# Performance work log

Hardware: AMD Instinct MI355X
Metric: run time of the kernel (lower is better)

Reference implementation:

```python
import jax, jax.numpy as jnp
import numpy as np

MIN_DISTANCE = 1.0  # default forward arg of the torch module


def setup_inputs() -> dict:
    key = jax.random.key(0)
    k1, k2 = jax.random.split(key)
    B, N = 4, 4096
    coords = jax.random.normal(k1, (B, N, 3), dtype=jnp.float32) * 5.0
    steric_radii = jax.random.uniform(k2, (B, N), dtype=jnp.float32)
    return {"coords": coords, "steric_radii": steric_radii}


def reference(coords, steric_radii):
    # coords: [B,N,3], steric_radii: [B,N]
    diff = coords[:, :, None, :] - coords[:, None, :, :]          # [B,N,N,3]
    d2 = jnp.sum(diff * diff, axis=-1)                             # [B,N,N]
    # safe sqrt: exact 0 on the diagonal (matches torch.cdist), no NaN grads
    pairwise = jnp.where(d2 > 0, jnp.sqrt(jnp.where(d2 > 0, d2, 1.0)), 0.0)
    sr = steric_radii[:, :, None] + steric_radii[:, None, :]       # [B,N,N]
    target = jnp.maximum(MIN_DISTANCE, sr)
    penalty = jax.nn.relu(target - pairwise)[..., None]            # [B,N,N,1]
    direction = jnp.clip(diff, -1.0, 1.0)                          # [B,N,N,3]
    adjustment = jnp.mean(penalty * direction, axis=2)             # [B,N,3]
    return coords + 0.1 * adjustment
```

## Files before the change

kernel.cpp:

```cpp
#include <hip/hip_runtime.h>

#define BB 4
#define NN 4096
#define TPB 1024
#define IBL 32
#define STREAMS 64
#define JPS (NN / STREAMS)
#define GRP 4

#if __has_builtin(__builtin_amdgcn_sqrtf)
  #define FAST_SQRT __builtin_amdgcn_sqrtf
#else
  #define FAST_SQRT sqrtf
#endif

__device__ __forceinline__ float clip1(float x) {
    return fminf(fmaxf(x, -1.0f), 1.0f);
}

__global__ __launch_bounds__(TPB, 8) void ncp_one(
    const float* __restrict__ coords,
    const float* __restrict__ radii,
    float* __restrict__ out)
{
    __shared__ __align__(16) char smem[81920];
    float4* pts = (float4*)smem;
    float*  rad = (float*)(smem + 65536);
    float*  red = (float*)smem;

    const int b = blockIdx.z;
    const int ibase = blockIdx.x * IBL;

    for (int p = threadIdx.x; p < NN; p += TPB) {
        const int g = b * NN + p;
        const float x = coords[3 * g + 0];
        const float y = coords[3 * g + 1];
        const float z = coords[3 * g + 2];
        pts[p] = make_float4(x, y, z, fmaf(z, z, fmaf(y, y, x * x)));
        rad[p] = radii[g];
    }
    __syncthreads();

    const int l = threadIdx.x & 63;
    const int li = l & 15;
    const int q  = l >> 4;
    const int w  = threadIdx.x >> 6;
    const int stream = w * 4 + q;
    const int jbase = stream * JPS;

    const float4 me0 = pts[ibase + li];
    const float4 me1 = pts[ibase + 16 + li];
    const float ri0 = rad[ibase + li];
    const float ri1 = rad[ibase + 16 + li];
    const float m2x0 = -2.0f * me0.x, m2y0 = -2.0f * me0.y, m2z0 = -2.0f * me0.z;
    const float m2x1 = -2.0f * me1.x, m2y1 = -2.0f * me1.y, m2z1 = -2.0f * me1.z;
    const float n20 = me0.w, n21 = me1.w;
    const float thr0 = (1.0f + ri0) * (1.0f + ri0) - n20;
    const float thr1 = (1.0f + ri1) * (1.0f + ri1) - n21;

    float ax0 = 0.0f, ay0 = 0.0f, az0 = 0.0f;
    float ax1 = 0.0f, ay1 = 0.0f, az1 = 0.0f;

    for (int k0 = 0; k0 < JPS; k0 += GRP) {
        float4 c[GRP];
        #pragma unroll
        for (int g = 0; g < GRP; ++g)
            c[g] = pts[jbase + k0 + g];
        #pragma unroll
        for (int g = 0; g < GRP; ++g) {
            const float sd0 = fmaf(m2z0, c[g].z,
                              fmaf(m2y0, c[g].y, fmaf(m2x0, c[g].x, c[g].w)));
            const float sd1 = fmaf(m2z1, c[g].z,
                              fmaf(m2y1, c[g].y, fmaf(m2x1, c[g].x, c[g].w)));
            if (__any(sd0 < thr0)) {
                const float rj   = rad[jbase + k0 + g];
                const float dist = FAST_SQRT(fmaxf(sd0 + n20, 0.0f));
                const float tgt  = fmaxf(1.0f, ri0 + rj);
                const float p    = fmaxf(tgt - dist, 0.0f);
                const float dx   = me0.x - c[g].x;
                const float dy   = me0.y - c[g].y;
                const float dz   = me0.z - c[g].z;
                ax0 = fmaf(p, clip1(dx), ax0);
                ay0 = fmaf(p, clip1(dy), ay0);
                az0 = fmaf(p, clip1(dz), az0);
            }
            if (__any(sd1 < thr1)) {
                const float rj   = rad[jbase + k0 + g];
                const float dist = FAST_SQRT(fmaxf(sd1 + n21, 0.0f));
                const float tgt  = fmaxf(1.0f, ri1 + rj);
                const float p    = fmaxf(tgt - dist, 0.0f);
                const float dx   = me1.x - c[g].x;
                const float dy   = me1.y - c[g].y;
                const float dz   = me1.z - c[g].z;
                ax1 = fmaf(p, clip1(dx), ax1);
                ay1 = fmaf(p, clip1(dy), ay1);
                az1 = fmaf(p, clip1(dz), az1);
            }
        }
    }

    __syncthreads();
    {
        const int r0 = (stream * IBL + li) * 3;
        const int r1 = (stream * IBL + 16 + li) * 3;
        red[r0 + 0] = ax0; red[r0 + 1] = ay0; red[r0 + 2] = az0;
        red[r1 + 0] = ax1; red[r1 + 1] = ay1; red[r1 + 2] = az1;
    }
    __syncthreads();

    if (threadIdx.x < IBL * 3) {
        float acc = 0.0f;
        #pragma unroll
        for (int s = 0; s < STREAMS; ++s)
            acc += red[s * (IBL * 3) + threadIdx.x];
        const int o = (b * NN + ibase) * 3 + threadIdx.x;
        out[o] = fmaf(0.1f / (float)NN, acc, coords[o]);
    }
}

extern "C" void kernel_launch(void* const* d_in, const int* in_sizes, int n_in,
                              void* d_out, int out_size, void* d_ws, size_t ws_size,
                              hipStream_t stream) {
    const float* coords = (const float*)d_in[0];
    const float* radii  = (const float*)d_in[1];
    float* out = (float*)d_out;
    (void)d_ws; (void)ws_size;

    ncp_one<<<dim3(NN / IBL, 1, BB), TPB, 0, stream>>>(coords, radii, out);
}
```

Before: 69.66 us.

## Register-block four i-points per thread with strided j-streams across 128 streams

Each thread now holds four i-points (8 lanes × 4) instead of two, and the j range is split into 128 interleaved streams with stride-128 access rather than contiguous chunks. Every j-point load from shared memory is reused across more i-points, and the 8 lanes of a group read the same address so the value is broadcast. The reduction buffer uses a padded stride of 100 to reduce LDS bank conflicts, and the direction vector is rebuilt from the -2x coefficients so the raw i coordinates need not stay in registers. The costs are more registers per thread, more partial sums to reduce, and coarser wave-wide __any branches, since each now covers 8 i-points × 8 streams.

```diff
diff --git a/kernel.cpp b/kernel.cpp
--- a/kernel.cpp
+++ b/kernel.cpp
@@ -4,9 +4,11 @@
 #define NN 4096
 #define TPB 1024
 #define IBL 32
-#define STREAMS 64
-#define JPS (NN / STREAMS)
-#define GRP 4
+#define IPT 4
+#define STREAMS 128
+#define JPT (NN / STREAMS)
+#define GRP 2
+#define RSTRIDE 100
 
 #if __has_builtin(__builtin_amdgcn_sqrtf)
   #define FAST_SQRT __builtin_amdgcn_sqrtf
@@ -41,80 +43,76 @@
     }
     __syncthreads();
 
-    const int l = threadIdx.x & 63;
-    const int li = l & 15;
-    const int q  = l >> 4;
+    const int l  = threadIdx.x & 63;
+    const int li = l & 7;
+    const int o  = l >> 3;
     const int w  = threadIdx.x >> 6;
-    const int stream = w * 4 + q;
-    const int jbase = stream * JPS;
+    const int s  = w * 8 + o;
 
-    const float4 me0 = pts[ibase + li];
-    const float4 me1 = pts[ibase + 16 + li];
-    const float ri0 = rad[ibase + li];
-    const float ri1 = rad[ibase + 16 + li];
-    const float m2x0 = -2.0f * me0.x, m2y0 = -2.0f * me0.y, m2z0 = -2.0f * me0.z;
-    const float m2x1 = -2.0f * me1.x, m2y1 = -2.0f * me1.y, m2z1 = -2.0f * me1.z;
-    const float n20 = me0.w, n21 = me1.w;
-    const float thr0 = (1.0f + ri0) * (1.0f + ri0) - n20;
-    const float thr1 = (1.0f + ri1) * (1.0f + ri1) - n21;
+    float m2x[IPT], m2y[IPT], m2z[IPT], thr[IPT], ri[IPT];
+    float ax[IPT], ay[IPT], az[IPT];
+    #pragma unroll
+    for (int t = 0; t < IPT; ++t) {
+        const float4 me = pts[ibase + li + 8 * t];
+        const float  r  = rad[ibase + li + 8 * t];
+        m2x[t] = -2.0f * me.x;
+        m2y[t] = -2.0f * me.y;
+        m2z[t] = -2.0f * me.z;
+        ri[t]  = r;
+        thr[t] = (1.0f + r) * (1.0f + r) - me.w;
+        ax[t] = 0.0f; ay[t] = 0.0f; az[t] = 0.0f;
+    }
 
-    float ax0 = 0.0f, ay0 = 0.0f, az0 = 0.0f;
-    float ax1 = 0.0f, ay1 = 0.0f, az1 = 0.0f;
+    const float4* __restrict__ pj = pts + s;
+    const float*  __restrict__ rj = rad + s;
 
-    for (int k0 = 0; k0 < JPS; k0 += GRP) {
+    for (int k0 = 0; k0 < JPT; k0 += GRP) {
         float4 c[GRP];
         #pragma unroll
         for (int g = 0; g < GRP; ++g)
-            c[g] = pts[jbase + k0 + g];
+            c[g] = pj[(k0 + g) * STREAMS];
         #pragma unroll
         for (int g = 0; g < GRP; ++g) {
-            const float sd0 = fmaf(m2z0, c[g].z,
-                              fmaf(m2y0, c[g].y, fmaf(m2x0, c[g].x, c[g].w)));
-            const float sd1 = fmaf(m2z1, c[g].z,
-                              fmaf(m2y1, c[g].y, fmaf(m2x1, c[g].x, c[g].w)));
-            if (__any(sd0 < thr0)) {
-                const float rj   = rad[jbase + k0 + g];
-                const float dist = FAST_SQRT(fmaxf(sd0 + n20, 0.0f));
-                const float tgt  = fmaxf(1.0f, ri0 + rj);
-                const float p    = fmaxf(tgt - dist, 0.0f);
-                const float dx   = me0.x - c[g].x;
-                const float dy   = me0.y - c[g].y;
-                const float dz   = me0.z - c[g].z;
-                ax0 = fmaf(p, clip1(dx), ax0);
-                ay0 = fmaf(p, clip1(dy), ay0);
-                az0 = fmaf(p, clip1(dz), az0);
-            }
-            if (__any(sd1 < thr1)) {
-                const float rj   = rad[jbase + k0 + g];
-                const float dist = FAST_SQRT(fmaxf(sd1 + n21, 0.0f));
-                const float tgt  = fmaxf(1.0f, ri1 + rj);
-                const float p    = fmaxf(tgt - dist, 0.0f);
-                const float dx   = me1.x - c[g].x;
-                const float dy   = me1.y - c[g].y;
-                const float dz   = me1.z - c[g].z;
-                ax1 = fmaf(p, clip1(dx), ax1);
-                ay1 = fmaf(p, clip1(dy), ay1);
-                az1 = fmaf(p, clip1(dz), az1);
+            #pragma unroll
+            for (int t = 0; t < IPT; ++t) {
+                const float sd = fmaf(m2z[t], c[g].z,
+                                 fmaf(m2y[t], c[g].y,
+                                 fmaf(m2x[t], c[g].x, c[g].w)));
+                if (__any(sd < thr[t])) {
+                    const float rjv  = rj[(k0 + g) * STREAMS];
+                    const float sp1  = 1.0f + ri[t];
+                    const float n2   = fmaf(sp1, sp1, -thr[t]);
+                    const float dist = FAST_SQRT(fmaxf(sd + n2, 0.0f));
+                    const float tgt  = fmaxf(1.0f, ri[t] + rjv);
+                    const float p    = fmaxf(tgt - dist, 0.0f);
+                    const float ex   = fmaf(0.5f, m2x[t], c[g].x);
+                    const float ey   = fmaf(0.5f, m2y[t], c[g].y);
+                    const float ez   = fmaf(0.5f, m2z[t], c[g].z);
+                    ax[t] = fmaf(p, -clip1(ex), ax[t]);
+                    ay[t] = fmaf(p, -clip1(ey), ay[t]);
+                    az[t] = fmaf(p, -clip1(ez), az[t]);
+                }
             }
         }
     }
 
     __syncthreads();
-    {
-        const int r0 = (stream * IBL + li) * 3;
-        const int r1 = (stream * IBL + 16 + li) * 3;
-        red[r0 + 0] = ax0; red[r0 + 1] = ay0; red[r0 + 2] = az0;
-        red[r1 + 0] = ax1; red[r1 + 1] = ay1; red[r1 + 2] = az1;
+    #pragma unroll
+    for (int t = 0; t < IPT; ++t) {
+        const int r0 = s * RSTRIDE + (li + 8 * t) * 3;
+        red[r0 + 0] = ax[t];
+        red[r0 + 1] = ay[t];
+        red[r0 + 2] = az[t];
     }
     __syncthreads();
 
     if (threadIdx.x < IBL * 3) {
         float acc = 0.0f;
-        #pragma unroll
-        for (int s = 0; s < STREAMS; ++s)
-            acc += red[s * (IBL * 3) + threadIdx.x];
-        const int o = (b * NN + ibase) * 3 + threadIdx.x;
-        out[o] = fmaf(0.1f / (float)NN, acc, coords[o]);
+        #pragma unroll 8
+        for (int ss = 0; ss < STREAMS; ++ss)
+            acc += red[ss * RSTRIDE + threadIdx.x];
+        const int oidx = (b * NN + ibase) * 3 + threadIdx.x;
+        out[oidx] = fmaf(0.1f / (float)NN, acc, coords[oidx]);
     }
 }
 
```

After: 69.17 us. Within noise of the previous version (-0.7%).
